# Optimization experiments

Hardware: AMD Instinct MI355X
Metric: run time of the kernel (lower is better)

## Reference

```python
import jax, jax.numpy as jnp
import numpy as np

N_NODES = 50000  # nodes in the (sub)graph


def setup_inputs() -> dict:
    key = jax.random.key(0)
    ks = jax.random.split(key, 8)
    nodes = jax.random.randint(ks[0], (N_NODES,), 0, 100000)
    src = jax.random.randint(ks[1], (800000,), 0, N_NODES)
    dst = jax.random.randint(ks[2], (800000,), 0, N_NODES)
    emb = jax.random.normal(ks[3], (100000, 256), dtype=jnp.float32)
    W = jax.random.normal(ks[4], (256, 128), dtype=jnp.float32) * 0.05
    b = jax.random.normal(ks[5], (128,), dtype=jnp.float32) * 0.05
    mlp_w = jax.random.normal(ks[6], (128, 40), dtype=jnp.float32) * 0.05
    mlp_b = jax.random.normal(ks[7], (40,), dtype=jnp.float32) * 0.05
    return {"nodes": nodes, "src": src, "dst": dst, "emb": emb,
            "W": W, "b": b, "mlp_w": mlp_w, "mlp_b": mlp_b}


def reference(nodes, src, dst, emb, W, b, mlp_w, mlp_b):
    n = N_NODES
    ones = jnp.ones_like(src, dtype=jnp.float32)
    out_deg = jax.ops.segment_sum(ones, src, num_segments=n)  # src out-degree
    in_deg = jax.ops.segment_sum(ones, dst, num_segments=n)   # dst in-degree
    norm_src = jax.lax.rsqrt(jnp.maximum(out_deg, 1.0))       # D_out^{-1/2}
    norm_dst = jax.lax.rsqrt(jnp.maximum(in_deg, 1.0))        # D_in^{-1/2}

    feat = emb[nodes]                                          # [N, in_dim]
    # dgl GraphConv(norm='both'): in_dim > out_dim -> project first, then aggregate
    h = (feat * norm_src[:, None]) @ W                         # [N, out_dim]
    agg = jax.ops.segment_sum(h[src], dst, num_segments=n)     # SpMM: sum over in-edges
    feat_out = agg * norm_dst[:, None] + b                     # [N, out_dim]

    logits = feat_out @ mlp_w + mlp_b                          # [N, num_classes]
    return (feat_out, logits)
```

## Files before the change

kernel.cpp:

```cpp
#include <hip/hip_runtime.h>

#define IN_DIM 256
#define OUT_DIM 128
#define N_CLS 40

#define SLICE 16384
#define NE_CH 40

typedef __attribute__((ext_vector_type(8))) short short8;
typedef __attribute__((ext_vector_type(4))) float floatx4;

static __device__ __forceinline__ unsigned short f2bf(float f) {
    union { float f; unsigned u; } v; v.f = f;
    unsigned r = v.u + 0x7FFF + ((v.u >> 16) & 1);
    return (unsigned short)(r >> 16);
}

static __device__ __forceinline__ unsigned cvtpk(float lo, float hi) {
    unsigned r;
    asm("v_cvt_pk_bf16_f32 %0, %1, %2" : "=v"(r) : "v"(lo), "v"(hi));
    return r;
}

__global__ __launch_bounds__(256) void hist_wconv_kernel(
    const int* __restrict__ src, const int* __restrict__ dst,
    int* __restrict__ partial_out, int* __restrict__ partial_in,
    const float* __restrict__ W, unsigned short* __restrict__ Wt,
    int ne, int n, int chunk, int nbh)
{
    __shared__ __align__(16) int lh_out[SLICE];
    __shared__ __align__(16) int lh_in[SLICE];

    const int tid = threadIdx.x;

    if (blockIdx.x >= nbh) {
        int t = (blockIdx.x - nbh) * 256 + tid;
        if (t < IN_DIM * OUT_DIM) {
            int k = t >> 7, c = t & 127;
            Wt[c * IN_DIM + k] = f2bf(W[t]);
        }
        return;
    }

    const int s = blockIdx.x / NE_CH;
    const int e = blockIdx.x % NE_CH;
    const int lo = s * SLICE;
    const int hi = min(lo + SLICE, n);

    for (int i = tid; i < SLICE; i += 256) { lh_out[i] = 0; lh_in[i] = 0; }
    __syncthreads();

    const int start = e * chunk;
    const int end = min(start + chunk, ne);
    const int cnt4 = (end - start) >> 2;
    const int4* s4 = (const int4*)(src + start);
    const int4* d4 = (const int4*)(dst + start);
    for (int k = tid; k < cnt4; k += 256) {
        int4 sv = s4[k];
        int4 dv = d4[k];
        unsigned q;
        q = (unsigned)(sv.x - lo); if (q < SLICE) atomicAdd(&lh_out[q], 1);
        q = (unsigned)(sv.y - lo); if (q < SLICE) atomicAdd(&lh_out[q], 1);
        q = (unsigned)(sv.z - lo); if (q < SLICE) atomicAdd(&lh_out[q], 1);
        q = (unsigned)(sv.w - lo); if (q < SLICE) atomicAdd(&lh_out[q], 1);
        q = (unsigned)(dv.x - lo); if (q < SLICE) atomicAdd(&lh_in[q], 1);
        q = (unsigned)(dv.y - lo); if (q < SLICE) atomicAdd(&lh_in[q], 1);
        q = (unsigned)(dv.z - lo); if (q < SLICE) atomicAdd(&lh_in[q], 1);
        q = (unsigned)(dv.w - lo); if (q < SLICE) atomicAdd(&lh_in[q], 1);
    }
    for (int t = start + (cnt4 << 2) + tid; t < end; t += 256) {
        unsigned q;
        q = (unsigned)(src[t] - lo); if (q < SLICE) atomicAdd(&lh_out[q], 1);
        q = (unsigned)(dst[t] - lo); if (q < SLICE) atomicAdd(&lh_in[q], 1);
    }
    __syncthreads();

    const int cnt = hi - lo;
    const int c4 = cnt >> 2;
    int4* po = (int4*)(partial_out + (size_t)e * n + lo);
    int4* pi = (int4*)(partial_in + (size_t)e * n + lo);
    for (int i = tid; i < c4; i += 256) {
        po[i] = ((const int4*)lh_out)[i];
        pi[i] = ((const int4*)lh_in)[i];
    }
    for (int i = (c4 << 2) + tid; i < cnt; i += 256) {
        partial_out[(size_t)e * n + lo + i] = lh_out[i];
        partial_in[(size_t)e * n + lo + i] = lh_in[i];
    }
}

__global__ __launch_bounds__(256) void reduce_scan_kernel(
    int* __restrict__ partial_out, int* __restrict__ partial_in,
    int* __restrict__ cnt_out, int* __restrict__ row_start,
    int* __restrict__ bsum, int n)
{
    __shared__ int wsum[4];
    const int tid = threadIdx.x;
    const int lane = tid & 63, wid = tid >> 6;
    const int base = blockIdx.x * 1024 + tid * 4;

    int4 run = make_int4(0, 0, 0, 0);

    if (base + 4 <= n) {
        int4 sum = make_int4(0, 0, 0, 0);
#pragma unroll
        for (int e = 0; e < NE_CH; e++) {
            int4 v = *(const int4*)(partial_out + (size_t)e * n + base);
            sum.x += v.x; sum.y += v.y; sum.z += v.z; sum.w += v.w;
        }
        *(int4*)(cnt_out + base) = sum;

#pragma unroll
        for (int e = 0; e < NE_CH; e++) {
            int* p = partial_in + (size_t)e * n + base;
            int4 v = *(const int4*)p;
            *(int4*)p = run;
            run.x += v.x; run.y += v.y; run.z += v.z; run.w += v.w;
        }
    } else if (base <= n) {
        int rr[4] = {0, 0, 0, 0};
#pragma unroll
        for (int j = 0; j < 4; j++) {
            int pos = base + j;
            if (pos < n) {
                int sum = 0, r = 0;
                for (int e = 0; e < NE_CH; e++) {
                    sum += partial_out[(size_t)e * n + pos];
                    int v = partial_in[(size_t)e * n + pos];
                    partial_in[(size_t)e * n + pos] = r;
                    r += v;
                }
                cnt_out[pos] = sum;
                rr[j] = r;
            }
        }
        run.x = rr[0]; run.y = rr[1]; run.z = rr[2]; run.w = rr[3];
    }

    const int s = run.x + run.y + run.z + run.w;
    const int e1 = run.x, e2 = run.x + run.y, e3 = run.x + run.y + run.z;

    int incl = s;
#pragma unroll
    for (int off = 1; off < 64; off <<= 1) {
        int q = __shfl_up(incl, (unsigned)off, 64);
        if (lane >= off) incl += q;
    }
    if (lane == 63) wsum[wid] = incl;
    __syncthreads();
    int woff = 0;
    for (int w = 0; w < wid; ++w) woff += wsum[w];
    const int texcl = woff + incl - s;

    if (base + 4 <= n) {
        int4 o = make_int4(texcl, texcl + e1, texcl + e2, texcl + e3);
        *(int4*)(row_start + base) = o;
    } else if (base <= n) {
        const int eo[4] = {0, e1, e2, e3};
#pragma unroll
        for (int j = 0; j < 4; j++) {
            int pos = base + j;
            if (pos <= n) row_start[pos] = texcl + eo[j];
        }
    }
    if (tid == 0) bsum[blockIdx.x] = wsum[0] + wsum[1] + wsum[2] + wsum[3];
}

__global__ __launch_bounds__(64) void scan2_kernel(
    const int* __restrict__ bsum, int* __restrict__ boffs, int nb)
{
    const int lane = threadIdx.x & 63;
    int carry = 0;
    for (int c = 0; c < nb; c += 64) {
        int i = c + lane;
        int v = (i < nb) ? bsum[i] : 0;
        int incl = v;
#pragma unroll
        for (int off = 1; off < 64; off <<= 1) {
            int q = __shfl_up(incl, (unsigned)off, 64);
            if (lane >= off) incl += q;
        }
        if (i < nb) boffs[i] = carry + incl - v;
        carry += __shfl(incl, 63, 64);
    }
    if (lane == 0) boffs[nb] = carry;
}

__global__ __launch_bounds__(256) void scatter_lds_kernel(
    const int* __restrict__ src, const int* __restrict__ dst,
    const int* __restrict__ row_start, const int* __restrict__ boffs,
    const int* __restrict__ prefix_in,
    int* __restrict__ csr_src, int ne, int n, int chunk)
{
    __shared__ __align__(16) int cur[SLICE];

    const int tid = threadIdx.x;
    const int s = blockIdx.x / NE_CH;
    const int e = blockIdx.x % NE_CH;
    const int lo = s * SLICE;
    const int hi = min(lo + SLICE, n);
    const int cnt = hi - lo;

    const int c4 = cnt >> 2;
    for (int i = tid; i < c4; i += 256) {
        int idx4 = lo + i * 4;
        int4 rs = *(const int4*)(row_start + idx4);
        int4 pf = *(const int4*)(prefix_in + (size_t)e * n + idx4);
        const int bo = boffs[idx4 >> 10];
        rs.x += pf.x + bo; rs.y += pf.y + bo;
        rs.z += pf.z + bo; rs.w += pf.w + bo;
        ((int4*)cur)[i] = rs;
    }
    for (int i = (c4 << 2) + tid; i < cnt; i += 256) {
        int pos = lo + i;
        cur[i] = row_start[pos] + boffs[pos >> 10]
               + prefix_in[(size_t)e * n + pos];
    }
    __syncthreads();

    const int start = e * chunk;
    const int end = min(start + chunk, ne);
    const int cnt4e = (end - start) >> 2;
    const int4* s4 = (const int4*)(src + start);
    const int4* d4 = (const int4*)(dst + start);
    for (int k = tid; k < cnt4e; k += 256) {
        int4 sv = s4[k];
        int4 dv = d4[k];
        unsigned q;
        q = (unsigned)(dv.x - lo); if (q < SLICE) csr_src[atomicAdd(&cur[q], 1)] = sv.x;
        q = (unsigned)(dv.y - lo); if (q < SLICE) csr_src[atomicAdd(&cur[q], 1)] = sv.y;
        q = (unsigned)(dv.z - lo); if (q < SLICE) csr_src[atomicAdd(&cur[q], 1)] = sv.z;
        q = (unsigned)(dv.w - lo); if (q < SLICE) csr_src[atomicAdd(&cur[q], 1)] = sv.w;
    }
    for (int t = start + (cnt4e << 2) + tid; t < end; t += 256) {
        unsigned q = (unsigned)(dst[t] - lo);
        if (q < SLICE) csr_src[atomicAdd(&cur[q], 1)] = src[t];
    }
}

__global__ __launch_bounds__(256) void gemm1_mfma_kernel(
    const int* __restrict__ nodes, const float* __restrict__ emb,
    const unsigned short* __restrict__ Wt, const int* __restrict__ cnt_out,
    unsigned short* __restrict__ h0, unsigned short* __restrict__ h1, int n)
{
    __shared__ unsigned short A_lds[128 * 40];
    __shared__ unsigned short B_lds[128 * 40];
    __shared__ int   snode[128];
    __shared__ float sscale[128];

    const int tid = threadIdx.x;
    const int m0  = blockIdx.x * 128;

    if (tid < 128) {
        int gr = m0 + tid;
        snode[tid]  = (gr < n) ? nodes[gr] : 0;
        sscale[tid] = (gr < n) ? rsqrtf(fmaxf((float)cnt_out[gr], 1.0f)) : 0.0f;
    }
    __syncthreads();

    const int arow = tid >> 1, aq = tid & 1;
    const float* aptr = emb + (size_t)snode[arow] * IN_DIM + aq * 16;
    const unsigned short* bptr = Wt + arow * IN_DIM + aq * 16;

    float    ar[16];
    unsigned bw[8];

#define LOAD_REGS(KK) do {                                           \
        _Pragma("unroll")                                            \
        for (int q = 0; q < 4; q++) {                                \
            const floatx4 v = *(const floatx4*)(aptr + (KK) * 32 + q * 4); \
            ar[q*4+0]=v[0]; ar[q*4+1]=v[1]; ar[q*4+2]=v[2]; ar[q*4+3]=v[3]; \
        }                                                            \
        const uint4 w0 = *(const uint4*)(bptr + (KK) * 32);          \
        const uint4 w1 = *(const uint4*)(bptr + (KK) * 32 + 8);      \
        bw[0]=w0.x; bw[1]=w0.y; bw[2]=w0.z; bw[3]=w0.w;              \
        bw[4]=w1.x; bw[5]=w1.y; bw[6]=w1.z; bw[7]=w1.w;              \
    } while (0)

#define WRITE_LDS() do {                                             \
        uint4 uv0, uv1;                                              \
        uv0.x = cvtpk(ar[0],  ar[1]);  uv0.y = cvtpk(ar[2],  ar[3]); \
        uv0.z = cvtpk(ar[4],  ar[5]);  uv0.w = cvtpk(ar[6],  ar[7]); \
        uv1.x = cvtpk(ar[8],  ar[9]);  uv1.y = cvtpk(ar[10], ar[11]);\
        uv1.z = cvtpk(ar[12], ar[13]); uv1.w = cvtpk(ar[14], ar[15]);\
        *(uint4*)&A_lds[arow * 40 + aq * 16]     = uv0;              \
        *(uint4*)&A_lds[arow * 40 + aq * 16 + 8] = uv1;              \
        uint4 b0, b1;                                                \
        b0.x=bw[0]; b0.y=bw[1]; b0.z=bw[2]; b0.w=bw[3];              \
        b1.x=bw[4]; b1.y=bw[5]; b1.z=bw[6]; b1.w=bw[7];              \
        *(uint4*)&B_lds[arow * 40 + aq * 16]     = b0;               \
        *(uint4*)&B_lds[arow * 40 + aq * 16 + 8] = b1;               \
    } while (0)

    const int wave = tid >> 6, lane = tid & 63;
    const int wr = (wave & 1) * 64;
    const int wc = (wave >> 1) * 64;
    const int fr = lane & 15;
    const int koff = (lane >> 4) * 8;

    floatx4 acc[4][4];
#pragma unroll
    for (int i = 0; i < 4; i++)
#pragma unroll
        for (int j = 0; j < 4; j++) acc[i][j] = (floatx4){0.f, 0.f, 0.f, 0.f};

    LOAD_REGS(0);
    WRITE_LDS();

    for (int kk = 0; kk < 8; ++kk) {
        if (kk < 7) LOAD_REGS(kk + 1);
        __syncthreads();
        short8 af[4], bf[4];
#pragma unroll
        for (int t = 0; t < 4; t++) {
            af[t] = *(const short8*)&A_lds[(wr + t * 16 + fr) * 40 + koff];
            bf[t] = *(const short8*)&B_lds[(wc + t * 16 + fr) * 40 + koff];
        }
#pragma unroll
        for (int rt = 0; rt < 4; rt++)
#pragma unroll
            for (int ct = 0; ct < 4; ct++)
                acc[rt][ct] = __builtin_amdgcn_mfma_f32_16x16x32_bf16(
                    bf[ct], af[rt], acc[rt][ct], 0, 0, 0);
        __syncthreads();
        if (kk < 7) WRITE_LDS();
    }

    unsigned short* hb = wc ? h1 : h0;
#pragma unroll
    for (int rt = 0; rt < 4; rt++) {
        int lrow = wr + rt * 16 + fr;
        int grow = m0 + lrow;
        float sc = sscale[lrow];
        if (grow < n) {
#pragma unroll
            for (int ct = 0; ct < 4; ct++) {
                int col = ct * 16 + (lane >> 4) * 4;
                uint2 o;
                o.x = cvtpk(acc[rt][ct][0] * sc, acc[rt][ct][1] * sc);
                o.y = cvtpk(acc[rt][ct][2] * sc, acc[rt][ct][3] * sc);
                *(uint2*)&hb[(size_t)grow * 64 + col] = o;
            }
        }
    }
#undef LOAD_REGS
#undef WRITE_LDS
}

__global__ __launch_bounds__(256) void spmm_half_kernel(
    const int* __restrict__ row_start, const int* __restrict__ boffs,
    const int* __restrict__ csr_src,
    const unsigned short* __restrict__ hh,
    const float* __restrict__ bias_half,
    float* __restrict__ out_col,
    int n)
{
    const int lane = threadIdx.x & 63;
    const int row = blockIdx.x * 4 + (threadIdx.x >> 6);
    if (row >= n) return;

    const int rs = row_start[row]     + boffs[row >> 10];
    const int re = row_start[row + 1] + boffs[(row + 1) >> 10];
    const int deg = re - rs;

    float a[4] = {0.f, 0.f, 0.f, 0.f};

    for (int base = 0; base < deg; base += 64) {
        const int cnt = min(deg - base, 64);
        int idx = (lane < cnt) ? csr_src[rs + base + lane] : 0;
        int t = 0;
        for (; t + 15 < cnt; t += 16) {
            int s[16];
#pragma unroll
            for (int u = 0; u < 16; u++) s[u] = __shfl(idx, t + u, 64);
            unsigned short v[16];
#pragma unroll
            for (int u = 0; u < 16; u++) v[u] = hh[(size_t)s[u] * 64 + lane];
#pragma unroll
            for (int u = 0; u < 16; u++) {
                union { unsigned uu; float f; } x;
                x.uu = ((unsigned)v[u]) << 16;
                a[u & 3] += x.f;
            }
        }
        for (; t + 3 < cnt; t += 4) {
            int s[4];
#pragma unroll
            for (int u = 0; u < 4; u++) s[u] = __shfl(idx, t + u, 64);
            unsigned short v[4];
#pragma unroll
            for (int u = 0; u < 4; u++) v[u] = hh[(size_t)s[u] * 64 + lane];
#pragma unroll
            for (int u = 0; u < 4; u++) {
                union { unsigned uu; float f; } x;
                x.uu = ((unsigned)v[u]) << 16;
                a[u] += x.f;
            }
        }
        for (; t < cnt; ++t) {
            int s0 = __shfl(idx, t, 64);
            union { unsigned uu; float f; } x;
            x.uu = ((unsigned)hh[(size_t)s0 * 64 + lane]) << 16;
            a[0] += x.f;
        }
    }

    const float nd = rsqrtf(fmaxf((float)deg, 1.0f));
    const float f0 = ((a[0] + a[1]) + (a[2] + a[3])) * nd + bias_half[lane];
    __builtin_nontemporal_store(f0, &out_col[(size_t)row * OUT_DIM + lane]);
}

__global__ __launch_bounds__(256) void mlp_mfma_kernel(
    const float* __restrict__ F, const float* __restrict__ mlp_w,
    const float* __restrict__ mlp_b, float* __restrict__ out_logits, int n)
{
    __shared__ unsigned short A_lds[48 * 136];
    __shared__ float s_mlpb[48];

    const int tid = threadIdx.x;
    for (int i = tid; i < 48 * 128; i += 256) {
        int cls = i >> 7, k = i & 127;
        A_lds[cls * 136 + k] =
            (cls < N_CLS) ? f2bf(mlp_w[(size_t)k * N_CLS + cls]) : (unsigned short)0;
    }
    if (tid < 48) s_mlpb[tid] = (tid < N_CLS) ? mlp_b[tid] : 0.f;
    __syncthreads();

    const int wave = tid >> 6, lane = tid & 63;
    const int r = lane & 15, koff = (lane >> 4) * 8;
    const int row = blockIdx.x * 64 + wave * 16 + r;
    const int rowc = (row < n) ? row : (n - 1);
    const float* fp = F + (size_t)rowc * OUT_DIM + koff;

    floatx4 acc[3];
#pragma unroll
    for (int ct = 0; ct < 3; ct++) acc[ct] = (floatx4){0.f, 0.f, 0.f, 0.f};

#pragma unroll
    for (int kk = 0; kk < 4; kk++) {
        floatx4 v0 = *(const floatx4*)(fp + kk * 32);
        floatx4 v1 = *(const floatx4*)(fp + kk * 32 + 4);
        union { unsigned u32[4]; short8 v; } bfr;
        bfr.u32[0] = cvtpk(v0[0], v0[1]);
        bfr.u32[1] = cvtpk(v0[2], v0[3]);
        bfr.u32[2] = cvtpk(v1[0], v1[1]);
        bfr.u32[3] = cvtpk(v1[2], v1[3]);
#pragma unroll
        for (int ct = 0; ct < 3; ct++) {
            short8 af = *(const short8*)&A_lds[(ct * 16 + r) * 136 + kk * 32 + koff];
            acc[ct] = __builtin_amdgcn_mfma_f32_16x16x32_bf16(af, bfr.v, acc[ct], 0, 0, 0);
        }
    }

    if (row < n) {
#pragma unroll
        for (int ct = 0; ct < 3; ct++)
#pragma unroll
            for (int i = 0; i < 4; i++) {
                int cls = ct * 16 + (lane >> 4) * 4 + i;
                if (cls < N_CLS)
                    __builtin_nontemporal_store(acc[ct][i] + s_mlpb[cls],
                        &out_logits[(size_t)row * N_CLS + cls]);
            }
    }
}

extern "C" void kernel_launch(void* const* d_in, const int* in_sizes, int n_in,
                              void* d_out, int out_size, void* d_ws, size_t ws_size,
                              hipStream_t stream) {
    const int*   nodes = (const int*)d_in[0];
    const int*   src   = (const int*)d_in[1];
    const int*   dst   = (const int*)d_in[2];
    const float* emb   = (const float*)d_in[3];
    const float* W     = (const float*)d_in[4];
    const float* b     = (const float*)d_in[5];
    const float* mlp_w = (const float*)d_in[6];
    const float* mlp_b = (const float*)d_in[7];

    const int n  = in_sizes[0];
    const int ne = in_sizes[1];

    int* cnt_out     = (int*)d_ws;
    int* bsum        = cnt_out + n;
    int* boffs       = bsum + 1024;
    int* row_start   = cnt_out + 2 * n;
    int* csr_src     = row_start + n + 8;
    int* partial_out = csr_src + ne;
    int* partial_in  = partial_out + (size_t)NE_CH * n;
    size_t off = ((size_t)(3 * n + 8) + (size_t)ne + 2 * (size_t)NE_CH * n) * sizeof(int);
    off = (off + 15) & ~(size_t)15;
    unsigned short* Wt = (unsigned short*)((char*)d_ws + off);
    off += (size_t)IN_DIM * OUT_DIM * sizeof(unsigned short);
    off = (off + 15) & ~(size_t)15;
    unsigned short* h0 = (unsigned short*)((char*)d_ws + off);
    unsigned short* h1 = h0 + (size_t)n * 64;

    float* out_feat   = (float*)d_out;
    float* out_logits = out_feat + (size_t)n * OUT_DIM;

    const int ns = (n + SLICE - 1) / SLICE;
    const int chunk = (((ne + NE_CH - 1) / NE_CH) + 3) & ~3;
    const int nbh = ns * NE_CH;
    const int nbw = (IN_DIM * OUT_DIM + 255) / 256;
    const int nb = (n + 1023) / 1024;

    hist_wconv_kernel<<<nbh + nbw, 256, 0, stream>>>(
        src, dst, partial_out, partial_in, W, Wt, ne, n, chunk, nbh);
    reduce_scan_kernel<<<nb, 256, 0, stream>>>(
        partial_out, partial_in, cnt_out, row_start, bsum, n);
    scan2_kernel<<<1, 64, 0, stream>>>(bsum, boffs, nb);
    scatter_lds_kernel<<<nbh, 256, 0, stream>>>(
        src, dst, row_start, boffs, partial_in, csr_src, ne, n, chunk);
    gemm1_mfma_kernel<<<(n + 127) / 128, 256, 0, stream>>>(
        nodes, emb, Wt, cnt_out, h0, h1, n);
    spmm_half_kernel<<<(n + 3) / 4, 256, 0, stream>>>(
        row_start, boffs, csr_src, h0, b, out_feat, n);
    spmm_half_kernel<<<(n + 3) / 4, 256, 0, stream>>>(
        row_start, boffs, csr_src, h1, b + 64, out_feat + 64, n);
    mlp_mfma_kernel<<<(n + 63) / 64, 256, 0, stream>>>(
        out_feat, mlp_w, mlp_b, out_logits, n);
}
```

Measured before the change: 146.2 us.

## Merge half SpMM kernels and fold block-offset scan into reduce kernel

Fuses the single-wave block-offset scan into the reduce/scan kernel using an atomic last-block-done pattern, removing one launch but adding a memset. Stores the projected features as one interleaved [n,128] bf16 buffer so a single SpMM pass gathers two columns per lane, halving CSR index traversal and doubling bytes per gather. Moves the GEMM launch ahead of the scatter kernel. Relies on threadfence/atomic ordering for correctness of the last-block scan.

```diff
diff --git a/kernel.cpp b/kernel.cpp
--- a/kernel.cpp
+++ b/kernel.cpp
@@ -92,9 +92,11 @@
 __global__ __launch_bounds__(256) void reduce_scan_kernel(
     int* __restrict__ partial_out, int* __restrict__ partial_in,
     int* __restrict__ cnt_out, int* __restrict__ row_start,
-    int* __restrict__ bsum, int n)
+    int* __restrict__ bsum, int* __restrict__ boffs,
+    int* __restrict__ done, int n)
 {
     __shared__ int wsum[4];
+    __shared__ int is_last;
     const int tid = threadIdx.x;
     const int lane = tid & 63, wid = tid >> 6;
     const int base = blockIdx.x * 1024 + tid * 4;
@@ -164,26 +166,31 @@
         }
     }
     if (tid == 0) bsum[blockIdx.x] = wsum[0] + wsum[1] + wsum[2] + wsum[3];
-}
-
-__global__ __launch_bounds__(64) void scan2_kernel(
-    const int* __restrict__ bsum, int* __restrict__ boffs, int nb)
-{
-    const int lane = threadIdx.x & 63;
-    int carry = 0;
-    for (int c = 0; c < nb; c += 64) {
-        int i = c + lane;
-        int v = (i < nb) ? bsum[i] : 0;
-        int incl = v;
-#pragma unroll
-        for (int off = 1; off < 64; off <<= 1) {
-            int q = __shfl_up(incl, (unsigned)off, 64);
-            if (lane >= off) incl += q;
-        }
-        if (i < nb) boffs[i] = carry + incl - v;
-        carry += __shfl(incl, 63, 64);
-    }
-    if (lane == 0) boffs[nb] = carry;
+
+    __threadfence();
+    if (tid == 0) {
+        int prev = atomicAdd(done, 1);
+        is_last = (prev == (int)gridDim.x - 1) ? 1 : 0;
+    }
+    __syncthreads();
+    if (is_last && tid < 64) {
+        __threadfence();
+        const int nb = (int)gridDim.x;
+        int carry = 0;
+        for (int c = 0; c < nb; c += 64) {
+            int i = c + lane;
+            int v = (i < nb) ? bsum[i] : 0;
+            int inc2 = v;
+#pragma unroll
+            for (int off = 1; off < 64; off <<= 1) {
+                int q = __shfl_up(inc2, (unsigned)off, 64);
+                if (lane >= off) inc2 += q;
+            }
+            if (i < nb) boffs[i] = carry + inc2 - v;
+            carry += __shfl(inc2, 63, 64);
+        }
+        if (lane == 0) boffs[nb] = carry;
+    }
 }
 
 __global__ __launch_bounds__(256) void scatter_lds_kernel(
@@ -241,7 +248,7 @@
 __global__ __launch_bounds__(256) void gemm1_mfma_kernel(
     const int* __restrict__ nodes, const float* __restrict__ emb,
     const unsigned short* __restrict__ Wt, const int* __restrict__ cnt_out,
-    unsigned short* __restrict__ h0, unsigned short* __restrict__ h1, int n)
+    unsigned short* __restrict__ h, int n)
 {
     __shared__ unsigned short A_lds[128 * 40];
     __shared__ unsigned short B_lds[128 * 40];
@@ -326,7 +333,6 @@
         if (kk < 7) WRITE_LDS();
     }
 
-    unsigned short* hb = wc ? h1 : h0;
 #pragma unroll
     for (int rt = 0; rt < 4; rt++) {
         int lrow = wr + rt * 16 + fr;
@@ -335,11 +341,11 @@
         if (grow < n) {
 #pragma unroll
             for (int ct = 0; ct < 4; ct++) {
-                int col = ct * 16 + (lane >> 4) * 4;
+                int col = wc + ct * 16 + (lane >> 4) * 4;
                 uint2 o;
                 o.x = cvtpk(acc[rt][ct][0] * sc, acc[rt][ct][1] * sc);
                 o.y = cvtpk(acc[rt][ct][2] * sc, acc[rt][ct][3] * sc);
-                *(uint2*)&hb[(size_t)grow * 64 + col] = o;
+                *(uint2*)&h[(size_t)grow * OUT_DIM + col] = o;
             }
         }
     }
@@ -347,15 +353,13 @@
 #undef WRITE_LDS
 }
 
-__global__ __launch_bounds__(256) void spmm_half_kernel(
+__global__ __launch_bounds__(256) void spmm_csr_kernel(
     const int* __restrict__ row_start, const int* __restrict__ boffs,
-    const int* __restrict__ csr_src,
-    const unsigned short* __restrict__ hh,
-    const float* __restrict__ bias_half,
-    float* __restrict__ out_col,
-    int n)
+    const int* __restrict__ csr_src, const unsigned short* __restrict__ h,
+    const float* __restrict__ bias, float* __restrict__ out_feat, int n)
 {
     const int lane = threadIdx.x & 63;
+    const int c2 = lane * 2;
     const int row = blockIdx.x * 4 + (threadIdx.x >> 6);
     if (row >= n) return;
 
@@ -363,7 +367,8 @@
     const int re = row_start[row + 1] + boffs[(row + 1) >> 10];
     const int deg = re - rs;
 
-    float a[4] = {0.f, 0.f, 0.f, 0.f};
+    float aL[4] = {0.f, 0.f, 0.f, 0.f};
+    float aH[4] = {0.f, 0.f, 0.f, 0.f};
 
     for (int base = 0; base < deg; base += 64) {
         const int cnt = min(deg - base, 64);
@@ -373,41 +378,54 @@
             int s[16];
 #pragma unroll
             for (int u = 0; u < 16; u++) s[u] = __shfl(idx, t + u, 64);
-            unsigned short v[16];
-#pragma unroll
-            for (int u = 0; u < 16; u++) v[u] = hh[(size_t)s[u] * 64 + lane];
+            unsigned v[16];
+#pragma unroll
+            for (int u = 0; u < 16; u++)
+                v[u] = *(const unsigned*)&h[(size_t)s[u] * OUT_DIM + c2];
 #pragma unroll
             for (int u = 0; u < 16; u++) {
-                union { unsigned uu; float f; } x;
-                x.uu = ((unsigned)v[u]) << 16;
-                a[u & 3] += x.f;
+                union { unsigned uu; float f; } x, y;
+                x.uu = v[u] << 16;
+                y.uu = v[u] & 0xffff0000u;
+                aL[u & 3] += x.f;
+                aH[u & 3] += y.f;
             }
         }
         for (; t + 3 < cnt; t += 4) {
             int s[4];
 #pragma unroll
             for (int u = 0; u < 4; u++) s[u] = __shfl(idx, t + u, 64);
-            unsigned short v[4];
-#pragma unroll
-            for (int u = 0; u < 4; u++) v[u] = hh[(size_t)s[u] * 64 + lane];
+            unsigned v[4];
+#pragma unroll
+            for (int u = 0; u < 4; u++)
+                v[u] = *(const unsigned*)&h[(size_t)s[u] * OUT_DIM + c2];
 #pragma unroll
             for (int u = 0; u < 4; u++) {
-                union { unsigned uu; float f; } x;
-                x.uu = ((unsigned)v[u]) << 16;
-                a[u] += x.f;
+                union { unsigned uu; float f; } x, y;
+                x.uu = v[u] << 16;
+                y.uu = v[u] & 0xffff0000u;
+                aL[u] += x.f;
+                aH[u] += y.f;
             }
         }
         for (; t < cnt; ++t) {
             int s0 = __shfl(idx, t, 64);
-            union { unsigned uu; float f; } x;
-            x.uu = ((unsigned)hh[(size_t)s0 * 64 + lane]) << 16;
-            a[0] += x.f;
+            unsigned v0 = *(const unsigned*)&h[(size_t)s0 * OUT_DIM + c2];
+            union { unsigned uu; float f; } x, y;
+            x.uu = v0 << 16;
+            y.uu = v0 & 0xffff0000u;
+            aL[0] += x.f;
+            aH[0] += y.f;
         }
     }
 
     const float nd = rsqrtf(fmaxf((float)deg, 1.0f));
-    const float f0 = ((a[0] + a[1]) + (a[2] + a[3])) * nd + bias_half[lane];
-    __builtin_nontemporal_store(f0, &out_col[(size_t)row * OUT_DIM + lane]);
+    const float f0 = ((aL[0] + aL[1]) + (aL[2] + aL[3])) * nd + bias[c2];
+    const float f1 = ((aH[0] + aH[1]) + (aH[2] + aH[3])) * nd + bias[c2 + 1];
+    union { float f[2]; unsigned long long u; } o;
+    o.f[0] = f0; o.f[1] = f1;
+    __builtin_nontemporal_store(o.u,
+        (unsigned long long*)&out_feat[(size_t)row * OUT_DIM + c2]);
 }
 
 __global__ __launch_bounds__(256) void mlp_mfma_kernel(
@@ -482,18 +500,18 @@
 
     int* cnt_out     = (int*)d_ws;
     int* bsum        = cnt_out + n;
-    int* boffs       = bsum + 1024;
-    int* row_start   = cnt_out + 2 * n;
+    int* boffs       = bsum + 512;
+    int* done        = boffs + 512;
+    int* row_start   = done + 8;
     int* csr_src     = row_start + n + 8;
     int* partial_out = csr_src + ne;
     int* partial_in  = partial_out + (size_t)NE_CH * n;
-    size_t off = ((size_t)(3 * n + 8) + (size_t)ne + 2 * (size_t)NE_CH * n) * sizeof(int);
+    size_t off = ((size_t)(2 * n + 1048) + (size_t)ne + 2 * (size_t)NE_CH * n) * sizeof(int);
     off = (off + 15) & ~(size_t)15;
     unsigned short* Wt = (unsigned short*)((char*)d_ws + off);
     off += (size_t)IN_DIM * OUT_DIM * sizeof(unsigned short);
     off = (off + 15) & ~(size_t)15;
-    unsigned short* h0 = (unsigned short*)((char*)d_ws + off);
-    unsigned short* h1 = h0 + (size_t)n * 64;
+    unsigned short* h = (unsigned short*)((char*)d_ws + off);
 
     float* out_feat   = (float*)d_out;
     float* out_logits = out_feat + (size_t)n * OUT_DIM;
@@ -504,19 +522,18 @@
     const int nbw = (IN_DIM * OUT_DIM + 255) / 256;
     const int nb = (n + 1023) / 1024;
 
+    hipMemsetAsync(done, 0, sizeof(int), stream);
+
     hist_wconv_kernel<<<nbh + nbw, 256, 0, stream>>>(
         src, dst, partial_out, partial_in, W, Wt, ne, n, chunk, nbh);
     reduce_scan_kernel<<<nb, 256, 0, stream>>>(
-        partial_out, partial_in, cnt_out, row_start, bsum, n);
-    scan2_kernel<<<1, 64, 0, stream>>>(bsum, boffs, nb);
+        partial_out, partial_in, cnt_out, row_start, bsum, boffs, done, n);
+    gemm1_mfma_kernel<<<(n + 127) / 128, 256, 0, stream>>>(
+        nodes, emb, Wt, cnt_out, h, n);
     scatter_lds_kernel<<<nbh, 256, 0, stream>>>(
         src, dst, row_start, boffs, partial_in, csr_src, ne, n, chunk);
-    gemm1_mfma_kernel<<<(n + 127) / 128, 256, 0, stream>>>(
-        nodes, emb, Wt, cnt_out, h0, h1, n);
-    spmm_half_kernel<<<(n + 3) / 4, 256, 0, stream>>>(
-        row_start, boffs, csr_src, h0, b, out_feat, n);
-    spmm_half_kernel<<<(n + 3) / 4, 256, 0, stream>>>(
-        row_start, boffs, csr_src, h1, b + 64, out_feat + 64, n);
+    spmm_csr_kernel<<<(n + 3) / 4, 256, 0, stream>>>(
+        row_start, boffs, csr_src, h, b, out_feat, n);
     mlp_mfma_kernel<<<(n + 63) / 64, 256, 0, stream>>>(
         out_feat, mlp_w, mlp_b, out_logits, n);
 }
```

After: 135.4 us. 7.4% less time.
